# Kernel tuning notes

Measured on AMD Instinct MI355X. Metric: run time of the kernel, lower is better.

The kernel has to match this reference:

```python
import jax, jax.numpy as jnp
import numpy as np

B, S, D = 2, 2048, 256
N_QK, N_V = 8192, 8192
NCPS = 32            # n_cells_per_side
MPC = 16             # max entries per cell -> 9*MPC = 144 candidates
MAX_K_QK, MAX_K_V = 32, 64
POS_MIN = jnp.array([-4.0, -4.0], dtype=jnp.float32)
POS_RANGE = jnp.array([8.0, 8.0], dtype=jnp.float32)
_OFF = jnp.array([[-1, -1], [-1, 0], [-1, 1], [0, -1], [0, 0], [0, 1], [1, -1], [1, 0], [1, 1]], dtype=jnp.int32)


def cell_lookup(query_pos, cell_map):
    # query_pos: [B,S,2], cell_map: [NCPS*NCPS, MPC] int32, -1 = padding
    Bq, Sq, _ = query_pos.shape
    mpc = cell_map.shape[1]
    normalized = (query_pos - POS_MIN) / POS_RANGE
    cell_xy = jnp.clip((normalized * NCPS).astype(jnp.int32), 0, NCPS - 1)
    nbr = jnp.clip(cell_xy[:, :, None, :] + _OFF[None, None, :, :], 0, NCPS - 1)  # [B,S,9,2]
    nbr_idx = nbr[..., 0] * NCPS + nbr[..., 1]                                     # [B,S,9]
    cand = cell_map[nbr_idx].reshape(Bq, Sq, 9 * mpc)
    valid = cand >= 0
    return jnp.where(valid, cand, 0), valid


def threshold_gate(scores, tau, max_k):
    raw = scores - tau
    gate = jnp.where(raw > 0, raw, 1e-8 * jnp.exp(raw))
    exp_gate = jnp.exp(gate) - 1.0
    k = min(max_k, scores.shape[-1])
    topv, _ = jax.lax.top_k(exp_gate, k)
    thr = topv[:, :, -1:]
    exp_gate = jnp.where(exp_gate >= thr, exp_gate, 0.0)
    gate_sum = exp_gate.sum(axis=-1, keepdims=True) + 1e-8
    strength = jnp.tanh(exp_gate.max(axis=-1, keepdims=True))
    return exp_gate / gate_sum * strength


def setup_inputs() -> dict:
    key = jax.random.key(0)
    ks = jax.random.split(key, 11)
    x = jax.random.normal(ks[0], (B, S, D), jnp.float32)
    qk_neurons = jax.random.normal(ks[1], (N_QK, D), jnp.float32) * 0.02
    v_neurons = jax.random.normal(ks[2], (N_V, D), jnp.float32) * 0.02
    neuron_pos = jax.random.normal(ks[3], (N_QK + N_V, 2), jnp.float32)
    W_pos_qk = jax.random.normal(ks[4], (D, 2), jnp.float32) * 0.05
    b_pos_qk = jnp.zeros((2,), jnp.float32)
    W_pos_v = jax.random.normal(ks[5], (D, 2), jnp.float32) * 0.05
    b_pos_v = jnp.zeros((2,), jnp.float32)
    W_tau = jax.random.normal(ks[6], (D, 3), jnp.float32) * 0.02
    b_tau = jnp.zeros((3,), jnp.float32)
    cm_qk = jax.random.randint(ks[7], (NCPS * NCPS, MPC), 0, N_QK)
    cm_qk = jnp.where(jax.random.bernoulli(ks[8], 0.15, cm_qk.shape), -1, cm_qk).astype(jnp.int32)
    cm_v = jax.random.randint(ks[9], (NCPS * NCPS, MPC), 0, N_V)
    cm_v = jnp.where(jax.random.bernoulli(ks[10], 0.15, cm_v.shape), -1, cm_v).astype(jnp.int32)
    return {"x": x, "qk_neurons": qk_neurons, "v_neurons": v_neurons, "neuron_pos": neuron_pos,
            "W_pos_qk": W_pos_qk, "b_pos_qk": b_pos_qk, "W_pos_v": W_pos_v, "b_pos_v": b_pos_v,
            "W_tau": W_tau, "b_tau": b_tau, "cell_map_qk": cm_qk, "cell_map_v": cm_v}


def reference(x, qk_neurons, v_neurons, neuron_pos, W_pos_qk, b_pos_qk, W_pos_v, b_pos_v, W_tau, b_tau, cell_map_qk, cell_map_v):
    qk_pos = x @ W_pos_qk + b_pos_qk        # [B,S,2]
    v_pos = x @ W_pos_v + b_pos_v
    ci_qk, m_qk = cell_lookup(qk_pos, cell_map_qk)   # [B,S,144]
    ci_v, m_v = cell_lookup(v_pos, cell_map_v)
    cand_qk = qk_neurons[ci_qk]             # [B,S,144,D] gather (dominant traffic)
    cand_v = v_neurons[ci_v]
    # dropout is deterministic (eval) -> identity; scores_Q == scores_K in source
    s_qk = jnp.where(m_qk, jnp.einsum('bsd,bsnd->bsn', x, cand_qk), -1e9)
    s_v = jnp.where(m_v, jnp.einsum('bsd,bsnd->bsn', x, cand_v), -1e9)
    tau = x @ W_tau + b_tau                 # [B,S,3]
    gQ = threshold_gate(s_qk, tau[:, :, 0:1], MAX_K_QK)
    gK = threshold_gate(s_qk, tau[:, :, 1:2], MAX_K_QK)
    gV = threshold_gate(s_v, tau[:, :, 2:3], MAX_K_V)
    npos_qk = neuron_pos[:N_QK]
    npos_v = neuron_pos[N_QK:N_QK + N_V]
    d_qk = jnp.sum((qk_pos[:, :, None, :] - npos_qk[ci_qk]) ** 2, axis=-1)
    d_v = jnp.sum((v_pos[:, :, None, :] - npos_v[ci_v]) ** 2, axis=-1)
    pos_loss = (jax.lax.stop_gradient(gQ) * d_qk * m_qk).sum() / (m_qk.sum() + 1e-8) \
             + (jax.lax.stop_gradient(gV) * d_v * m_v).sum() / (m_v.sum() + 1e-8)
    return jnp.stack([gQ, gK, gV]), pos_loss
```

## Files before the change

kernel.cpp:

```cpp
#include <hip/hip_runtime.h>
#include <math.h>

#define BB 2
#define SS 2048
#define DD 256
#define NTOK (BB * SS)
#define N_QK 8192
#define N_V  8192
#define NCPS 32
#define MPC  16
#define NC   144
#define K_QK 32
#define K_V  64
#define OUT_GATES (3 * NTOK * NC)

__global__ __launch_bounds__(256) void router_main(
    const float* __restrict__ x,
    const float* __restrict__ qk_neurons,
    const float* __restrict__ v_neurons,
    const float* __restrict__ neuron_pos,
    const float* __restrict__ W_pos_qk, const float* __restrict__ b_pos_qk,
    const float* __restrict__ W_pos_v,  const float* __restrict__ b_pos_v,
    const float* __restrict__ W_tau,    const float* __restrict__ b_tau,
    const int* __restrict__ cm_qk, const int* __restrict__ cm_v,
    float* __restrict__ out, float* __restrict__ ws)
{
    const int token = blockIdx.x;
    const int tid   = threadIdx.x;
    const int lane  = tid & 63, wid = tid >> 6;

    __shared__ __align__(16) float  x_s[DD];
    __shared__ float  scal[8];
    __shared__ double partd[4][7];
    __shared__ int    ci_s[2][NC];
    __shared__ float  sc_s[2][NC];
    __shared__ float  d_s[2][NC];
    __shared__ __align__(16) float eg3[3][NC];
    __shared__ float  tc3[3][NC];

    float xv = x[(size_t)token * DD + tid];
    x_s[tid] = xv;
    double p[7];
    p[0] = (double)xv * (double)W_pos_qk[tid * 2 + 0];
    p[1] = (double)xv * (double)W_pos_qk[tid * 2 + 1];
    p[2] = (double)xv * (double)W_pos_v[tid * 2 + 0];
    p[3] = (double)xv * (double)W_pos_v[tid * 2 + 1];
    p[4] = (double)xv * (double)W_tau[tid * 3 + 0];
    p[5] = (double)xv * (double)W_tau[tid * 3 + 1];
    p[6] = (double)xv * (double)W_tau[tid * 3 + 2];
    #pragma unroll
    for (int j = 0; j < 7; ++j) {
        double v = p[j];
        for (int o = 32; o; o >>= 1) v += __shfl_down(v, o, 64);
        p[j] = v;
    }
    if (lane == 0) {
        #pragma unroll
        for (int j = 0; j < 7; ++j) partd[wid][j] = p[j];
    }
    __syncthreads();
    if (tid < 7) {
        double v = partd[0][tid] + partd[1][tid] + partd[2][tid] + partd[3][tid];
        float bias = (tid < 2) ? b_pos_qk[tid]
                   : (tid < 4) ? b_pos_v[tid - 2]
                               : b_tau[tid - 4];
        scal[tid] = (float)v + bias;
    }
    __syncthreads();

    for (int c = tid; c < 2 * NC; c += 256) {
        int side = (c >= NC);
        int n    = side ? c - NC : c;
        float px = scal[side * 2 + 0], py = scal[side * 2 + 1];
        int cx = (int)(((px + 4.0f) / 8.0f) * 32.0f);
        int cy = (int)(((py + 4.0f) / 8.0f) * 32.0f);
        cx = min(max(cx, 0), NCPS - 1);
        cy = min(max(cy, 0), NCPS - 1);
        int o = n / MPC, slot = n % MPC;
        int nx = min(max(cx + (o / 3 - 1), 0), NCPS - 1);
        int ny = min(max(cy + (o % 3 - 1), 0), NCPS - 1);
        int idx = nx * NCPS + ny;
        int cand = (side ? cm_v : cm_qk)[idx * MPC + slot];
        ci_s[side][n] = cand;
        const float* npos = neuron_pos + (side ? (size_t)N_QK * 2 : 0);
        int cidx = max(cand, 0);
        float dx = px - npos[cidx * 2 + 0];
        float dy = py - npos[cidx * 2 + 1];
        d_s[side][n] = dx * dx + dy * dy;
    }
    __syncthreads();

    {
        const int quad = tid >> 2, ql = tid & 3;
        const float4* x4 = (const float4*)x_s;
        for (int c = quad; c < 2 * NC; c += 64) {
            int side = (c >= NC);
            int n    = side ? c - NC : c;
            int cand = ci_s[side][n];
            const float4* row = (const float4*)((side ? v_neurons : qk_neurons)
                                                + (size_t)max(cand, 0) * DD);
            double ax = 0.0, ay = 0.0, az = 0.0, aw = 0.0;
            #pragma unroll
            for (int i = ql; i < 64; i += 4) {
                float4 r  = row[i];
                float4 xx = x4[i];
                ax = fma((double)r.x, (double)xx.x, ax);
                ay = fma((double)r.y, (double)xx.y, ay);
                az = fma((double)r.z, (double)xx.z, az);
                aw = fma((double)r.w, (double)xx.w, aw);
            }
            double acc = (ax + ay) + (az + aw);
            acc += __shfl_xor(acc, 1, 64);
            acc += __shfl_xor(acc, 2, 64);
            if (ql == 0)
                sc_s[side][n] = (cand >= 0) ? (float)acc : -1e9f;
        }
    }
    __syncthreads();

    for (int idx = tid; idx < 3 * NC; idx += 256) {
        int g = (idx >= 2 * NC) ? 2 : (idx >= NC ? 1 : 0);
        int j = idx - g * NC;
        float s   = sc_s[g == 2][j];
        float raw = s - scal[4 + g];
        float gate = (raw > 0.0f) ? raw : 1e-8f * expf(raw);
        eg3[g][j] = expf(gate) - 1.0f;
    }
    __syncthreads();

    for (int idx = tid; idx < 3 * NC; idx += 256) {
        int g = (idx >= 2 * NC) ? 2 : (idx >= NC ? 1 : 0);
        int j = idx - g * NC;
        float my = eg3[g][j];
        const float4* e4 = (const float4*)&eg3[g][0];
        int cnt = 0;
        #pragma unroll
        for (int q = 0; q < NC / 4; ++q) {
            float4 e = e4[q];
            cnt += (e.x > my) + (e.y > my) + (e.z > my) + (e.w > my);
        }
        int k = (g == 2) ? K_V : K_QK;
        tc3[g][j] = (cnt < k) ? my : 3.402823466e38f;
    }
    __syncthreads();

    if (wid < 3) {
        const int g = wid, side = (g == 2);
        const bool has2 = (lane < 16);
        float e0 = eg3[g][lane],       e1 = eg3[g][lane + 64];
        float t0 = tc3[g][lane],       t1 = tc3[g][lane + 64];
        float e2 = has2 ? eg3[g][lane + 128] : 0.0f;
        float t2 = has2 ? tc3[g][lane + 128] : 3.402823466e38f;
        float mn = fminf(fminf(t0, t1), t2);
        float mx = fmaxf(fmaxf(e0, e1), e2);
        #pragma unroll
        for (int o = 32; o; o >>= 1) {
            mn = fminf(mn, __shfl_xor(mn, o, 64));
            mx = fmaxf(mx, __shfl_xor(mx, o, 64));
        }
        const float thr = mn;
        float k0 = (e0 >= thr) ? e0 : 0.0f;
        float k1 = (e1 >= thr) ? e1 : 0.0f;
        float k2 = (has2 && e2 >= thr) ? e2 : 0.0f;
        float sum = k0 + k1 + k2;
        #pragma unroll
        for (int o = 32; o; o >>= 1) sum += __shfl_xor(sum, o, 64);
        const float gs = sum + 1e-8f;
        const float strength = tanhf(mx);
        float o0 = k0 / gs * strength;
        float o1 = k1 / gs * strength;
        float o2 = k2 / gs * strength;
        float* og = out + ((size_t)g * NTOK + token) * NC;
        og[lane]      = o0;
        og[lane + 64] = o1;
        if (has2) og[lane + 128] = o2;

        if (g != 1) {
            float m0 = (ci_s[side][lane]       >= 0) ? 1.0f : 0.0f;
            float m1 = (ci_s[side][lane + 64]  >= 0) ? 1.0f : 0.0f;
            float m2 = (has2 && ci_s[side][lane + 128] >= 0) ? 1.0f : 0.0f;
            float w = o0 * d_s[side][lane] * m0 + o1 * d_s[side][lane + 64] * m1;
            if (has2) w += o2 * d_s[side][lane + 128] * m2;
            float c = m0 + m1 + m2;
            #pragma unroll
            for (int o = 32; o; o >>= 1) {
                w += __shfl_xor(w, o, 64);
                c += __shfl_xor(c, o, 64);
            }
            if (lane == 0) {
                ws[(size_t)token * 4 + (side ? 2 : 0)] = w;
                ws[(size_t)token * 4 + (side ? 3 : 1)] = c;
            }
        }
    }
}

__global__ __launch_bounds__(1024) void router_finalize(
    const float* __restrict__ ws, float* __restrict__ out)
{
    __shared__ double red[16][4];
    const int t = threadIdx.x, lane = t & 63, w = t >> 6;
    double wq = 0, cq = 0, wv = 0, cv = 0;
    const float4* w4 = (const float4*)ws;
    for (int i = t; i < NTOK; i += 1024) {
        float4 v = w4[i];
        wq += (double)v.x; cq += (double)v.y;
        wv += (double)v.z; cv += (double)v.w;
    }
    for (int o = 32; o; o >>= 1) {
        wq += __shfl_down(wq, o, 64);
        cq += __shfl_down(cq, o, 64);
        wv += __shfl_down(wv, o, 64);
        cv += __shfl_down(cv, o, 64);
    }
    if (lane == 0) { red[w][0] = wq; red[w][1] = cq; red[w][2] = wv; red[w][3] = cv; }
    __syncthreads();
    if (t == 0) {
        double a = 0, b = 0, c = 0, d = 0;
        for (int i = 0; i < 16; ++i) {
            a += red[i][0]; b += red[i][1]; c += red[i][2]; d += red[i][3];
        }
        out[OUT_GATES] = (float)(a / (b + 1e-8) + c / (d + 1e-8));
    }
}

extern "C" void kernel_launch(void* const* d_in, const int* in_sizes, int n_in,
                              void* d_out, int out_size, void* d_ws, size_t ws_size,
                              hipStream_t stream) {
    const float* x          = (const float*)d_in[0];
    const float* qk_neurons = (const float*)d_in[1];
    const float* v_neurons  = (const float*)d_in[2];
    const float* neuron_pos = (const float*)d_in[3];
    const float* W_pos_qk   = (const float*)d_in[4];
    const float* b_pos_qk   = (const float*)d_in[5];
    const float* W_pos_v    = (const float*)d_in[6];
    const float* b_pos_v    = (const float*)d_in[7];
    const float* W_tau      = (const float*)d_in[8];
    const float* b_tau      = (const float*)d_in[9];
    const int*   cm_qk      = (const int*)d_in[10];
    const int*   cm_v       = (const int*)d_in[11];

    float* out = (float*)d_out;
    float* ws  = (float*)d_ws;

    router_main<<<NTOK, 256, 0, stream>>>(
        x, qk_neurons, v_neurons, neuron_pos,
        W_pos_qk, b_pos_qk, W_pos_v, b_pos_v, W_tau, b_tau,
        cm_qk, cm_v, out, ws);
    router_finalize<<<1, 1024, 0, stream>>>(ws, out);
}
```

Before: 199.1 us.

## Fuse finalize into main via last-block atomic and restructure candidate dot products

Drops the separate finalize kernel: the last block to finish, found with a global atomic counter reset by a memset, does the pos_loss reduction. The gather dot product now gives each candidate row to 16 lanes instead of 4, so loads within a row are more contiguous. Top-k rank counting runs on raw scores for two sides instead of three gated arrays, relying on the gate being monotone, and the threshold is mapped through the gate afterwards. This removes one barrier and one pass, but adds a memset launch and threadfence/atomic overhead.

```diff
diff --git a/kernel.cpp b/kernel.cpp
--- a/kernel.cpp
+++ b/kernel.cpp
@@ -13,6 +13,7 @@
 #define K_QK 32
 #define K_V  64
 #define OUT_GATES (3 * NTOK * NC)
+#define WS_COUNTER_OFF (4 * NTOK)
 
 __global__ __launch_bounds__(256) void router_main(
     const float* __restrict__ x,
@@ -33,18 +34,22 @@
     __shared__ float  scal[8];
     __shared__ double partd[4][7];
     __shared__ int    ci_s[2][NC];
-    __shared__ float  sc_s[2][NC];
+    __shared__ __align__(16) float sc_s[2][NC];
     __shared__ float  d_s[2][NC];
     __shared__ __align__(16) float eg3[3][NC];
-    __shared__ float  tc3[3][NC];
+    __shared__ float  tc2[2][NC];
+    __shared__ int    flag_s;
+    __shared__ double redd[4][4];
 
     float xv = x[(size_t)token * DD + tid];
     x_s[tid] = xv;
+    float2 wqk = ((const float2*)W_pos_qk)[tid];
+    float2 wv2 = ((const float2*)W_pos_v)[tid];
     double p[7];
-    p[0] = (double)xv * (double)W_pos_qk[tid * 2 + 0];
-    p[1] = (double)xv * (double)W_pos_qk[tid * 2 + 1];
-    p[2] = (double)xv * (double)W_pos_v[tid * 2 + 0];
-    p[3] = (double)xv * (double)W_pos_v[tid * 2 + 1];
+    p[0] = (double)xv * (double)wqk.x;
+    p[1] = (double)xv * (double)wqk.y;
+    p[2] = (double)xv * (double)wv2.x;
+    p[3] = (double)xv * (double)wv2.y;
     p[4] = (double)xv * (double)W_tau[tid * 3 + 0];
     p[5] = (double)xv * (double)W_tau[tid * 3 + 1];
     p[6] = (double)xv * (double)W_tau[tid * 3 + 2];
@@ -91,66 +96,69 @@
     __syncthreads();
 
     {
-        const int quad = tid >> 2, ql = tid & 3;
+        const int sub = lane >> 4;
+        const int c   = lane & 15;
+        const int rowbase = wid * 72;
         const float4* x4 = (const float4*)x_s;
-        for (int c = quad; c < 2 * NC; c += 64) {
-            int side = (c >= NC);
-            int n    = side ? c - NC : c;
+        #pragma unroll 2
+        for (int g = 0; g < 18; ++g) {
+            int r    = rowbase + g * 4 + sub;
+            int side = (r >= NC);
+            int n    = r - side * NC;
             int cand = ci_s[side][n];
             const float4* row = (const float4*)((side ? v_neurons : qk_neurons)
                                                 + (size_t)max(cand, 0) * DD);
             double ax = 0.0, ay = 0.0, az = 0.0, aw = 0.0;
             #pragma unroll
-            for (int i = ql; i < 64; i += 4) {
-                float4 r  = row[i];
-                float4 xx = x4[i];
-                ax = fma((double)r.x, (double)xx.x, ax);
-                ay = fma((double)r.y, (double)xx.y, ay);
-                az = fma((double)r.z, (double)xx.z, az);
-                aw = fma((double)r.w, (double)xx.w, aw);
+            for (int k = 0; k < 4; ++k) {
+                float4 rr = row[c + 16 * k];
+                float4 xx = x4[c + 16 * k];
+                ax = fma((double)rr.x, (double)xx.x, ax);
+                ay = fma((double)rr.y, (double)xx.y, ay);
+                az = fma((double)rr.z, (double)xx.z, az);
+                aw = fma((double)rr.w, (double)xx.w, aw);
             }
             double acc = (ax + ay) + (az + aw);
             acc += __shfl_xor(acc, 1, 64);
             acc += __shfl_xor(acc, 2, 64);
-            if (ql == 0)
-                sc_s[side][n] = (cand >= 0) ? (float)acc : -1e9f;
+            acc += __shfl_xor(acc, 4, 64);
+            acc += __shfl_xor(acc, 8, 64);
+            if (c == 0) sc_s[side][n] = (cand >= 0) ? (float)acc : -1e9f;
         }
     }
     __syncthreads();
 
     for (int idx = tid; idx < 3 * NC; idx += 256) {
-        int g = (idx >= 2 * NC) ? 2 : (idx >= NC ? 1 : 0);
+        int g = (idx >= 2 * NC) ? 2 : (idx >= NC);
         int j = idx - g * NC;
         float s   = sc_s[g == 2][j];
         float raw = s - scal[4 + g];
         float gate = (raw > 0.0f) ? raw : 1e-8f * expf(raw);
         eg3[g][j] = expf(gate) - 1.0f;
     }
-    __syncthreads();
-
-    for (int idx = tid; idx < 3 * NC; idx += 256) {
-        int g = (idx >= 2 * NC) ? 2 : (idx >= NC ? 1 : 0);
-        int j = idx - g * NC;
-        float my = eg3[g][j];
-        const float4* e4 = (const float4*)&eg3[g][0];
+    for (int idx = tid; idx < 2 * NC; idx += 256) {
+        int side = (idx >= NC);
+        int n    = idx - side * NC;
+        float my = sc_s[side][n];
+        const float4* s4 = (const float4*)&sc_s[side][0];
         int cnt = 0;
         #pragma unroll
         for (int q = 0; q < NC / 4; ++q) {
-            float4 e = e4[q];
+            float4 e = s4[q];
             cnt += (e.x > my) + (e.y > my) + (e.z > my) + (e.w > my);
         }
-        int k = (g == 2) ? K_V : K_QK;
-        tc3[g][j] = (cnt < k) ? my : 3.402823466e38f;
+        int k = side ? K_V : K_QK;
+        tc2[side][n] = (cnt < k) ? my : 3.402823466e38f;
     }
     __syncthreads();
 
     if (wid < 3) {
         const int g = wid, side = (g == 2);
         const bool has2 = (lane < 16);
-        float e0 = eg3[g][lane],       e1 = eg3[g][lane + 64];
-        float t0 = tc3[g][lane],       t1 = tc3[g][lane + 64];
+        float t0 = tc2[side][lane], t1 = tc2[side][lane + 64];
+        float t2 = has2 ? tc2[side][lane + 128] : 3.402823466e38f;
+        float e0 = eg3[g][lane],   e1 = eg3[g][lane + 64];
         float e2 = has2 ? eg3[g][lane + 128] : 0.0f;
-        float t2 = has2 ? tc3[g][lane + 128] : 3.402823466e38f;
         float mn = fminf(fminf(t0, t1), t2);
         float mx = fmaxf(fmaxf(e0, e1), e2);
         #pragma unroll
@@ -158,7 +166,10 @@
             mn = fminf(mn, __shfl_xor(mn, o, 64));
             mx = fmaxf(mx, __shfl_xor(mx, o, 64));
         }
-        const float thr = mn;
+        float rawk  = mn - scal[4 + g];
+        float gatek = (rawk > 0.0f) ? rawk : 1e-8f * expf(rawk);
+        float thr   = expf(gatek) - 1.0f;
+
         float k0 = (e0 >= thr) ? e0 : 0.0f;
         float k1 = (e1 >= thr) ? e1 : 0.0f;
         float k2 = (has2 && e2 >= thr) ? e2 : 0.0f;
@@ -193,34 +204,40 @@
             }
         }
     }
-}
-
-__global__ __launch_bounds__(1024) void router_finalize(
-    const float* __restrict__ ws, float* __restrict__ out)
-{
-    __shared__ double red[16][4];
-    const int t = threadIdx.x, lane = t & 63, w = t >> 6;
-    double wq = 0, cq = 0, wv = 0, cv = 0;
-    const float4* w4 = (const float4*)ws;
-    for (int i = t; i < NTOK; i += 1024) {
-        float4 v = w4[i];
-        wq += (double)v.x; cq += (double)v.y;
-        wv += (double)v.z; cv += (double)v.w;
-    }
-    for (int o = 32; o; o >>= 1) {
-        wq += __shfl_down(wq, o, 64);
-        cq += __shfl_down(cq, o, 64);
-        wv += __shfl_down(wv, o, 64);
-        cv += __shfl_down(cv, o, 64);
-    }
-    if (lane == 0) { red[w][0] = wq; red[w][1] = cq; red[w][2] = wv; red[w][3] = cv; }
-    __syncthreads();
-    if (t == 0) {
-        double a = 0, b = 0, c = 0, d = 0;
-        for (int i = 0; i < 16; ++i) {
-            a += red[i][0]; b += red[i][1]; c += red[i][2]; d += red[i][3];
-        }
-        out[OUT_GATES] = (float)(a / (b + 1e-8) + c / (d + 1e-8));
+    __syncthreads();
+
+    if (tid == 0) {
+        __threadfence();
+        unsigned old = atomicAdd((unsigned*)(ws + WS_COUNTER_OFF), 1u);
+        flag_s = (old == NTOK - 1);
+    }
+    __syncthreads();
+    if (flag_s) {
+        __threadfence();
+        double wq = 0, cq = 0, wv = 0, cv = 0;
+        const float4* w4 = (const float4*)ws;
+        for (int i = tid; i < NTOK; i += 256) {
+            float4 v = w4[i];
+            wq += (double)v.x; cq += (double)v.y;
+            wv += (double)v.z; cv += (double)v.w;
+        }
+        #pragma unroll
+        for (int o = 32; o; o >>= 1) {
+            wq += __shfl_down(wq, o, 64);
+            cq += __shfl_down(cq, o, 64);
+            wv += __shfl_down(wv, o, 64);
+            cv += __shfl_down(cv, o, 64);
+        }
+        if (lane == 0) { redd[wid][0] = wq; redd[wid][1] = cq; redd[wid][2] = wv; redd[wid][3] = cv; }
+        __syncthreads();
+        if (tid == 0) {
+            double a = 0, b = 0, c = 0, d = 0;
+            #pragma unroll
+            for (int i = 0; i < 4; ++i) {
+                a += redd[i][0]; b += redd[i][1]; c += redd[i][2]; d += redd[i][3];
+            }
+            out[OUT_GATES] = (float)(a / (b + 1e-8) + c / (d + 1e-8));
+        }
     }
 }
 
@@ -243,9 +260,10 @@
     float* out = (float*)d_out;
     float* ws  = (float*)d_ws;
 
+    hipMemsetAsync(ws + WS_COUNTER_OFF, 0, sizeof(unsigned), stream);
+
     router_main<<<NTOK, 256, 0, stream>>>(
         x, qk_neurons, v_neurons, neuron_pos,
         W_pos_qk, b_pos_qk, W_pos_v, b_pos_v, W_tau, b_tau,
         cm_qk, cm_v, out, ws);
-    router_finalize<<<1, 1024, 0, stream>>>(ws, out);
 }
```

Measured after the change: 288.3 us. 44.8% more time.
